# Optimization experiments

Hardware: AMD Instinct MI355X
Metric: run time of the kernel (lower is better)

The kernel has to match this reference:

```python
import jax, jax.numpy as jnp
import numpy as np

B, NQ, NK, D = 8, 2048, 2048, 1024

def setup_inputs() -> dict:
    key = jax.random.key(0)
    k1, k2, k3, k4, k5 = jax.random.split(key, 5)
    query_input = jax.random.normal(k1, (B, NQ, D), dtype=jnp.float32)
    key_input = jax.random.normal(k2, (B, NK, D), dtype=jnp.float32)
    s = 1.0 / np.sqrt(D)
    # nn.Linear(in,out,bias=False): y = x @ W.T, W shape (out,in)
    Wq = jax.random.uniform(k3, (D, D), dtype=jnp.float32, minval=-s, maxval=s)
    Wk = jax.random.uniform(k4, (D, D), dtype=jnp.float32, minval=-s, maxval=s)
    Wv = jax.random.uniform(k5, (D, D), dtype=jnp.float32, minval=-s, maxval=s)
    return {"query_input": query_input, "key_input": key_input,
            "Wq": Wq, "Wk": Wk, "Wv": Wv}

def reference(query_input, key_input, Wq, Wk, Wv):
    d = query_input.shape[-1]
    q = jnp.einsum('bnd,ed->bne', query_input, Wq)   # (b, n_q, d)
    k = jnp.einsum('bmd,ed->bme', key_input, Wk)     # (b, n_k, d)
    v = jnp.einsum('bnd,ed->bne', query_input, Wv)   # (b, n_q, d) -- value from query_input
    # scores: K @ Q^T -> (b, n_k, n_q), softmax over n_q
    a = jnp.einsum('bmd,bnd->bmn', k, q) / jnp.sqrt(jnp.float32(d))
    a = jax.nn.softmax(a, axis=-1)
    context = jnp.einsum('bmn,bnd->bmd', a, v)       # (b, n_k, d)
    return context + key_input
```

## Files before the change

### kernel.cpp

```cpp
#include <hip/hip_runtime.h>
#include <hip/hip_bf16.h>

using bf16 = __bf16;
typedef __bf16 bf16x8 __attribute__((ext_vector_type(8)));
typedef float f32x4 __attribute__((ext_vector_type(4)));

__device__ __forceinline__ void gload_lds16(const bf16* g, bf16* l) {
  __builtin_amdgcn_global_load_lds(
      (const __attribute__((address_space(1))) void*)g,
      (__attribute__((address_space(3))) void*)l, 16, 0, 0);
}

__global__ __launch_bounds__(256) void cvt_f32_bf16(const float* __restrict__ in,
                                                    bf16* __restrict__ out, int n) {
  int i = (blockIdx.x * 256 + threadIdx.x) * 8;
  if (i >= n) return;
  float4 f0 = *(const float4*)&in[i];
  float4 f1 = *(const float4*)&in[i + 4];
  bf16x8 o;
  o[0] = (bf16)f0.x; o[1] = (bf16)f0.y; o[2] = (bf16)f0.z; o[3] = (bf16)f0.w;
  o[4] = (bf16)f1.x; o[5] = (bf16)f1.y; o[6] = (bf16)f1.z; o[7] = (bf16)f1.w;
  *(bf16x8*)&out[i] = o;
}

template <int EPI>
__global__ __launch_bounds__(512, 2)
void gemm_bt(const bf16* __restrict__ A, const bf16* __restrict__ B,
             void* __restrict__ Cv, const float* __restrict__ Add,
             int K, int lda, int ldb, int ldc,
             long sA, long sB, long sC, long sAdd, float scale) {
  const int z = blockIdx.z;
  A += (long)z * sA;
  B += (long)z * sB;
  const int tid = threadIdx.x;
  const int lane = tid & 63;
  const int wave = tid >> 6;
  const int wr = wave >> 2;
  const int wc = wave & 3;
  const long brow = (long)blockIdx.x * 256;
  const long bcol = (long)blockIdx.y * 256;

  __shared__ bf16 lds[4][16384];

  f32x4 acc[8][4] = {};

  const int srow = tid >> 2;
  const int scg  = (tid & 3) ^ ((srow >> 1) & 3);
  const bf16* gA = A + (brow + srow) * (long)lda + scg * 8;
  const bf16* gB = B + (bcol + srow) * (long)ldb + scg * 8;
  const long a128 = (long)lda << 7;
  const long b128 = (long)ldb << 7;

  const int nk = K >> 5;

  auto stageA = [&](int t) {
    bf16* buf = lds[t & 3];
    const bf16* g = gA + (long)t * 32;
    gload_lds16(g,        buf + tid * 8);
    gload_lds16(g + a128, buf + 4096 + tid * 8);
  };
  auto stageB = [&](int t) {
    bf16* buf = lds[t & 3];
    const bf16* g = gB + (long)t * 32;
    gload_lds16(g,        buf + 8192 + tid * 8);
    gload_lds16(g + b128, buf + 12288 + tid * 8);
  };

  stageA(0); stageB(0);
  stageA(1); stageB(1);
  stageA(2); stageB(2);
  asm volatile("s_waitcnt vmcnt(8)" ::: "memory");
  __builtin_amdgcn_s_barrier();

  const int lk = lane >> 4;
  const int lr = lane & 15;

  for (int t = 0; t < nk; ++t) {
    bf16* buf = lds[t & 3];
    bf16x8 av[8], bv[4];
#pragma unroll
    for (int mi = 0; mi < 4; ++mi) {
      const int r = wr * 128 + mi * 16 + lr;
      av[mi] = *(const bf16x8*)&buf[r * 32 + ((lk ^ ((r >> 1) & 3)) << 3)];
    }
#pragma unroll
    for (int ni = 0; ni < 4; ++ni) {
      const int r = wc * 64 + ni * 16 + lr;
      bv[ni] = *(const bf16x8*)&buf[8192 + r * 32 + ((lk ^ ((r >> 1) & 3)) << 3)];
    }
    if (t + 3 < nk) stageA(t + 3);
    __builtin_amdgcn_s_setprio(1);
#pragma unroll
    for (int mi = 0; mi < 4; ++mi)
#pragma unroll
      for (int ni = 0; ni < 4; ++ni)
        acc[mi][ni] = __builtin_amdgcn_mfma_f32_16x16x32_bf16(av[mi], bv[ni],
                                                              acc[mi][ni], 0, 0, 0);
    __builtin_amdgcn_s_setprio(0);
    __builtin_amdgcn_s_barrier();
#pragma unroll
    for (int mi = 4; mi < 8; ++mi) {
      const int r = wr * 128 + mi * 16 + lr;
      av[mi] = *(const bf16x8*)&buf[r * 32 + ((lk ^ ((r >> 1) & 3)) << 3)];
    }
    if (t + 3 < nk) stageB(t + 3);
    __builtin_amdgcn_s_setprio(1);
#pragma unroll
    for (int mi = 4; mi < 8; ++mi)
#pragma unroll
      for (int ni = 0; ni < 4; ++ni)
        acc[mi][ni] = __builtin_amdgcn_mfma_f32_16x16x32_bf16(av[mi], bv[ni],
                                                              acc[mi][ni], 0, 0, 0);
    __builtin_amdgcn_s_setprio(0);
    if (t < nk - 3)       { asm volatile("s_waitcnt vmcnt(8)" ::: "memory"); }
    else if (t == nk - 3) { asm volatile("s_waitcnt vmcnt(4)" ::: "memory"); }
    else if (t == nk - 2) { asm volatile("s_waitcnt vmcnt(0)" ::: "memory"); }
    __builtin_amdgcn_s_barrier();
  }

  const int or0 = wr * 128 + ((lane >> 4) << 2);
  const int oc0 = wc * 64 + (lane & 15);
#pragma unroll
  for (int mi = 0; mi < 8; ++mi) {
#pragma unroll
    for (int ni = 0; ni < 4; ++ni) {
#pragma unroll
      for (int j = 0; j < 4; ++j) {
        const long row = brow + or0 + mi * 16 + j;
        const long col = bcol + oc0 + ni * 16;
        const float vres = acc[mi][ni][j] * scale;
        if constexpr (EPI == 0) {
          bf16* C = (bf16*)Cv + (long)z * sC;
          C[row * ldc + col] = (bf16)vres;
        } else {
          float* C = (float*)Cv + (long)z * sC;
          const float* Ad = Add + (long)z * sAdd;
          C[row * ldc + col] = vres + Ad[row * ldc + col];
        }
      }
    }
  }
}

__global__ __launch_bounds__(256) void softmax_rows(bf16* __restrict__ S) {
  const long row = blockIdx.x;
  bf16* p = S + row * 2048;
  const int tid = threadIdx.x;
  bf16x8 v = *(const bf16x8*)&p[tid * 8];
  float x[8];
  float m = -1e30f;
#pragma unroll
  for (int i = 0; i < 8; ++i) { x[i] = (float)v[i]; m = fmaxf(m, x[i]); }
#pragma unroll
  for (int off = 32; off > 0; off >>= 1) m = fmaxf(m, __shfl_xor(m, off, 64));
  __shared__ float red[4];
  __shared__ float red2[4];
  if ((tid & 63) == 0) red[tid >> 6] = m;
  __syncthreads();
  m = fmaxf(fmaxf(red[0], red[1]), fmaxf(red[2], red[3]));
  float e[8];
  float s = 0.f;
#pragma unroll
  for (int i = 0; i < 8; ++i) { e[i] = __expf(x[i] - m); s += e[i]; }
#pragma unroll
  for (int off = 32; off > 0; off >>= 1) s += __shfl_xor(s, off, 64);
  if ((tid & 63) == 0) red2[tid >> 6] = s;
  __syncthreads();
  s = red2[0] + red2[1] + red2[2] + red2[3];
  const float inv = 1.0f / s;
  bf16x8 o;
#pragma unroll
  for (int i = 0; i < 8; ++i) o[i] = (bf16)(e[i] * inv);
  *(bf16x8*)&p[tid * 8] = o;
}

extern "C" void kernel_launch(void* const* d_in, const int* in_sizes, int n_in,
                              void* d_out, int out_size, void* d_ws, size_t ws_size,
                              hipStream_t stream) {
  const float* q_in = (const float*)d_in[0];
  const float* k_in = (const float*)d_in[1];
  const float* Wq   = (const float*)d_in[2];
  const float* Wk   = (const float*)d_in[3];
  const float* Wv   = (const float*)d_in[4];
  float* out = (float*)d_out;
  char* ws = (char*)d_ws;

  bf16* qb  = (bf16*)(ws);
  bf16* kb  = (bf16*)(ws + 33554432);
  bf16* S   = (bf16*)(ws);
  bf16* Wqb = (bf16*)(ws + 67108864);
  bf16* Wkb = (bf16*)(ws + 69206016);
  bf16* Wvb = (bf16*)(ws + 71303168);
  bf16* Qp  = (bf16*)(ws + 73400320);
  bf16* Kp  = (bf16*)(ws + 106954752);
  bf16* Vpt = (bf16*)(ws + 140509184);

  cvt_f32_bf16<<<8192, 256, 0, stream>>>(q_in, qb, 16777216);
  cvt_f32_bf16<<<8192, 256, 0, stream>>>(k_in, kb, 16777216);
  cvt_f32_bf16<<<512, 256, 0, stream>>>(Wq, Wqb, 1048576);
  cvt_f32_bf16<<<512, 256, 0, stream>>>(Wk, Wkb, 1048576);
  cvt_f32_bf16<<<512, 256, 0, stream>>>(Wv, Wvb, 1048576);

  gemm_bt<0><<<dim3(64, 4, 1), 512, 0, stream>>>(
      qb, Wqb, Qp, nullptr, 1024, 1024, 1024, 1024, 0, 0, 0, 0, 1.0f);
  gemm_bt<0><<<dim3(64, 4, 1), 512, 0, stream>>>(
      kb, Wkb, Kp, nullptr, 1024, 1024, 1024, 1024, 0, 0, 0, 0, 1.0f);
  gemm_bt<0><<<dim3(4, 8, 8), 512, 0, stream>>>(
      Wvb, qb, Vpt, nullptr, 1024, 1024, 1024, 2048,
      0L, 2097152L, 2097152L, 0L, 1.0f);

  gemm_bt<0><<<dim3(8, 8, 8), 512, 0, stream>>>(
      Kp, Qp, S, nullptr, 1024, 1024, 1024, 2048,
      2097152L, 2097152L, 4194304L, 0L, 0.03125f);

  softmax_rows<<<16384, 256, 0, stream>>>(S);

  gemm_bt<2><<<dim3(8, 4, 8), 512, 0, stream>>>(
      S, Vpt, out, k_in, 2048, 2048, 2048, 1024,
      4194304L, 2097152L, 2097152L, 2097152L, 1.0f);
}
```

Before: 340.0 us.

## Fuse exp into score GEMM, defer softmax normalization, reschedule GEMM main loop

The score GEMM epilogue now writes exp(scaled score) directly with no max subtraction. A light row-sum kernel computes reciprocal sums, and the final GEMM multiplies by that inverse in its epilogue, so the separate softmax pass no longer rereads and rewrites S. The GEMM main loop is split into four finer LDS-read/MFMA phases with interleaved async loads, extra barriers and sched_barriers. Batched grids also get an XCD-aware block remap. Dropping the max subtraction risks overflow and precision loss if scores are large, and the extra barriers may add sync overhead.

After: 341.9 us. About the same (+0.6%).

```diff
diff --git a/kernel.cpp b/kernel.cpp
--- a/kernel.cpp
+++ b/kernel.cpp
@@ -27,18 +27,27 @@
 __global__ __launch_bounds__(512, 2)
 void gemm_bt(const bf16* __restrict__ A, const bf16* __restrict__ B,
              void* __restrict__ Cv, const float* __restrict__ Add,
+             const float* __restrict__ Inv,
              int K, int lda, int ldb, int ldc,
              long sA, long sB, long sC, long sAdd, float scale) {
-  const int z = blockIdx.z;
-  A += (long)z * sA;
-  B += (long)z * sB;
+  int bx = blockIdx.x, by = blockIdx.y, bz = blockIdx.z;
+  if (gridDim.z > 1) {
+    const int gx = gridDim.x, gxy = gx * gridDim.y;
+    const int nwg = gxy * gridDim.z;
+    int lin = bx + gx * by + gxy * bz;
+    lin = (lin & 7) * (nwg >> 3) + (lin >> 3);
+    bz = lin / gxy; const int rem = lin - bz * gxy;
+    by = rem / gx;  bx = rem - by * gx;
+  }
+  A += (long)bz * sA;
+  B += (long)bz * sB;
   const int tid = threadIdx.x;
   const int lane = tid & 63;
   const int wave = tid >> 6;
   const int wr = wave >> 2;
   const int wc = wave & 3;
-  const long brow = (long)blockIdx.x * 256;
-  const long bcol = (long)blockIdx.y * 256;
+  const long brow = (long)bx * 256;
+  const long bcol = (long)by * 256;
 
   __shared__ bf16 lds[4][16384];
 
@@ -53,64 +62,84 @@
 
   const int nk = K >> 5;
 
-  auto stageA = [&](int t) {
-    bf16* buf = lds[t & 3];
-    const bf16* g = gA + (long)t * 32;
-    gload_lds16(g,        buf + tid * 8);
-    gload_lds16(g + a128, buf + 4096 + tid * 8);
-  };
-  auto stageB = [&](int t) {
-    bf16* buf = lds[t & 3];
-    const bf16* g = gB + (long)t * 32;
-    gload_lds16(g,        buf + 8192 + tid * 8);
-    gload_lds16(g + b128, buf + 12288 + tid * 8);
-  };
-
-  stageA(0); stageB(0);
-  stageA(1); stageB(1);
-  stageA(2); stageB(2);
+  auto stageAlo = [&](int t) { gload_lds16(gA + (long)t * 32,        lds[t & 3] + tid * 8); };
+  auto stageAhi = [&](int t) { gload_lds16(gA + a128 + (long)t * 32, lds[t & 3] + 4096 + tid * 8); };
+  auto stageBlo = [&](int t) { gload_lds16(gB + (long)t * 32,        lds[t & 3] + 8192 + tid * 8); };
+  auto stageBhi = [&](int t) { gload_lds16(gB + b128 + (long)t * 32, lds[t & 3] + 12288 + tid * 8); };
+
+  stageAlo(0); stageAhi(0); stageBlo(0); stageBhi(0);
+  stageAlo(1); stageAhi(1); stageBlo(1); stageBhi(1);
+  stageAlo(2); stageAhi(2); stageBlo(2); stageBhi(2);
   asm volatile("s_waitcnt vmcnt(8)" ::: "memory");
   __builtin_amdgcn_s_barrier();
 
   const int lk = lane >> 4;
   const int lr = lane & 15;
+
+  auto rdA = [&](const bf16* buf, int mi) -> bf16x8 {
+    const int r = wr * 128 + mi * 16 + lr;
+    return *(const bf16x8*)&buf[r * 32 + ((lk ^ ((r >> 1) & 3)) << 3)];
+  };
+  auto rdB = [&](const bf16* buf, int ni) -> bf16x8 {
+    const int r = wc * 64 + ni * 16 + lr;
+    return *(const bf16x8*)&buf[8192 + r * 32 + ((lk ^ ((r >> 1) & 3)) << 3)];
+  };
 
   for (int t = 0; t < nk; ++t) {
     bf16* buf = lds[t & 3];
     bf16x8 av[8], bv[4];
 #pragma unroll
-    for (int mi = 0; mi < 4; ++mi) {
-      const int r = wr * 128 + mi * 16 + lr;
-      av[mi] = *(const bf16x8*)&buf[r * 32 + ((lk ^ ((r >> 1) & 3)) << 3)];
-    }
-#pragma unroll
-    for (int ni = 0; ni < 4; ++ni) {
-      const int r = wc * 64 + ni * 16 + lr;
-      bv[ni] = *(const bf16x8*)&buf[8192 + r * 32 + ((lk ^ ((r >> 1) & 3)) << 3)];
-    }
-    if (t + 3 < nk) stageA(t + 3);
+    for (int mi = 0; mi < 4; ++mi) av[mi] = rdA(buf, mi);
+#pragma unroll
+    for (int ni = 0; ni < 2; ++ni) bv[ni] = rdB(buf, ni);
+    if (t + 3 < nk) stageAlo(t + 3);
+    __builtin_amdgcn_s_barrier();
+    asm volatile("s_waitcnt lgkmcnt(0)" ::: "memory");
+    __builtin_amdgcn_sched_barrier(0);
     __builtin_amdgcn_s_setprio(1);
 #pragma unroll
     for (int mi = 0; mi < 4; ++mi)
 #pragma unroll
-      for (int ni = 0; ni < 4; ++ni)
-        acc[mi][ni] = __builtin_amdgcn_mfma_f32_16x16x32_bf16(av[mi], bv[ni],
-                                                              acc[mi][ni], 0, 0, 0);
-    __builtin_amdgcn_s_setprio(0);
-    __builtin_amdgcn_s_barrier();
-#pragma unroll
-    for (int mi = 4; mi < 8; ++mi) {
-      const int r = wr * 128 + mi * 16 + lr;
-      av[mi] = *(const bf16x8*)&buf[r * 32 + ((lk ^ ((r >> 1) & 3)) << 3)];
-    }
-    if (t + 3 < nk) stageB(t + 3);
+      for (int ni = 0; ni < 2; ++ni)
+        acc[mi][ni] = __builtin_amdgcn_mfma_f32_16x16x32_bf16(av[mi], bv[ni], acc[mi][ni], 0, 0, 0);
+    __builtin_amdgcn_s_setprio(0);
+    __builtin_amdgcn_s_barrier();
+#pragma unroll
+    for (int ni = 2; ni < 4; ++ni) bv[ni] = rdB(buf, ni);
+    if (t + 3 < nk) stageAhi(t + 3);
+    __builtin_amdgcn_s_barrier();
+    asm volatile("s_waitcnt lgkmcnt(0)" ::: "memory");
+    __builtin_amdgcn_sched_barrier(0);
+    __builtin_amdgcn_s_setprio(1);
+#pragma unroll
+    for (int mi = 0; mi < 4; ++mi)
+#pragma unroll
+      for (int ni = 2; ni < 4; ++ni)
+        acc[mi][ni] = __builtin_amdgcn_mfma_f32_16x16x32_bf16(av[mi], bv[ni], acc[mi][ni], 0, 0, 0);
+    __builtin_amdgcn_s_setprio(0);
+    __builtin_amdgcn_s_barrier();
+#pragma unroll
+    for (int mi = 4; mi < 8; ++mi) av[mi] = rdA(buf, mi);
+    if (t + 3 < nk) stageBlo(t + 3);
+    __builtin_amdgcn_s_barrier();
+    asm volatile("s_waitcnt lgkmcnt(0)" ::: "memory");
+    __builtin_amdgcn_sched_barrier(0);
     __builtin_amdgcn_s_setprio(1);
 #pragma unroll
     for (int mi = 4; mi < 8; ++mi)
 #pragma unroll
-      for (int ni = 0; ni < 4; ++ni)
-        acc[mi][ni] = __builtin_amdgcn_mfma_f32_16x16x32_bf16(av[mi], bv[ni],
-                                                              acc[mi][ni], 0, 0, 0);
+      for (int ni = 2; ni < 4; ++ni)
+        acc[mi][ni] = __builtin_amdgcn_mfma_f32_16x16x32_bf16(av[mi], bv[ni], acc[mi][ni], 0, 0, 0);
+    __builtin_amdgcn_s_setprio(0);
+    __builtin_amdgcn_s_barrier();
+    if (t + 3 < nk) stageBhi(t + 3);
+    __builtin_amdgcn_s_barrier();
+    __builtin_amdgcn_s_setprio(1);
+#pragma unroll
+    for (int mi = 4; mi < 8; ++mi)
+#pragma unroll
+      for (int ni = 0; ni < 2; ++ni)
+        acc[mi][ni] = __builtin_amdgcn_mfma_f32_16x16x32_bf16(av[mi], bv[ni], acc[mi][ni], 0, 0, 0);
     __builtin_amdgcn_s_setprio(0);
     if (t < nk - 3)       { asm volatile("s_waitcnt vmcnt(8)" ::: "memory"); }
     else if (t == nk - 3) { asm volatile("s_waitcnt vmcnt(4)" ::: "memory"); }
@@ -128,50 +157,38 @@
       for (int j = 0; j < 4; ++j) {
         const long row = brow + or0 + mi * 16 + j;
         const long col = bcol + oc0 + ni * 16;
-        const float vres = acc[mi][ni][j] * scale;
         if constexpr (EPI == 0) {
-          bf16* C = (bf16*)Cv + (long)z * sC;
-          C[row * ldc + col] = (bf16)vres;
+          bf16* C = (bf16*)Cv + (long)bz * sC;
+          C[row * ldc + col] = (bf16)(acc[mi][ni][j] * scale);
+        } else if constexpr (EPI == 1) {
+          bf16* C = (bf16*)Cv + (long)bz * sC;
+          C[row * ldc + col] = (bf16)__expf(acc[mi][ni][j] * scale);
         } else {
-          float* C = (float*)Cv + (long)z * sC;
-          const float* Ad = Add + (long)z * sAdd;
-          C[row * ldc + col] = vres + Ad[row * ldc + col];
+          float* C = (float*)Cv + (long)bz * sC;
+          const float* Ad = Add + (long)bz * sAdd;
+          const float* iv = Inv + (long)bz * 2048;
+          C[row * ldc + col] = acc[mi][ni][j] * iv[row] + Ad[row * ldc + col];
         }
       }
     }
   }
 }
 
-__global__ __launch_bounds__(256) void softmax_rows(bf16* __restrict__ S) {
+__global__ __launch_bounds__(256) void rowsum_inv(const bf16* __restrict__ E,
+                                                  float* __restrict__ inv) {
   const long row = blockIdx.x;
-  bf16* p = S + row * 2048;
+  const bf16* p = E + row * 2048;
   const int tid = threadIdx.x;
   bf16x8 v = *(const bf16x8*)&p[tid * 8];
-  float x[8];
-  float m = -1e30f;
-#pragma unroll
-  for (int i = 0; i < 8; ++i) { x[i] = (float)v[i]; m = fmaxf(m, x[i]); }
-#pragma unroll
-  for (int off = 32; off > 0; off >>= 1) m = fmaxf(m, __shfl_xor(m, off, 64));
+  float s = 0.f;
+#pragma unroll
+  for (int i = 0; i < 8; ++i) s += (float)v[i];
+#pragma unroll
+  for (int off = 32; off > 0; off >>= 1) s += __shfl_xor(s, off, 64);
   __shared__ float red[4];
-  __shared__ float red2[4];
-  if ((tid & 63) == 0) red[tid >> 6] = m;
+  if ((tid & 63) == 0) red[tid >> 6] = s;
   __syncthreads();
-  m = fmaxf(fmaxf(red[0], red[1]), fmaxf(red[2], red[3]));
-  float e[8];
-  float s = 0.f;
-#pragma unroll
-  for (int i = 0; i < 8; ++i) { e[i] = __expf(x[i] - m); s += e[i]; }
-#pragma unroll
-  for (int off = 32; off > 0; off >>= 1) s += __shfl_xor(s, off, 64);
-  if ((tid & 63) == 0) red2[tid >> 6] = s;
-  __syncthreads();
-  s = red2[0] + red2[1] + red2[2] + red2[3];
-  const float inv = 1.0f / s;
-  bf16x8 o;
-#pragma unroll
-  for (int i = 0; i < 8; ++i) o[i] = (bf16)(e[i] * inv);
-  *(bf16x8*)&p[tid * 8] = o;
+  if (tid == 0) inv[row] = 1.0f / (red[0] + red[1] + red[2] + red[3]);
 }
 
 extern "C" void kernel_launch(void* const* d_in, const int* in_sizes, int n_in,
@@ -189,6 +206,7 @@
   bf16* kb  = (bf16*)(ws + 33554432);
   bf16* S   = (bf16*)(ws);
   bf16* Wqb = (bf16*)(ws + 67108864);
+  float* inv = (float*)(ws + 67108864);
   bf16* Wkb = (bf16*)(ws + 69206016);
   bf16* Wvb = (bf16*)(ws + 71303168);
   bf16* Qp  = (bf16*)(ws + 73400320);
@@ -202,20 +220,20 @@
   cvt_f32_bf16<<<512, 256, 0, stream>>>(Wv, Wvb, 1048576);
 
   gemm_bt<0><<<dim3(64, 4, 1), 512, 0, stream>>>(
-      qb, Wqb, Qp, nullptr, 1024, 1024, 1024, 1024, 0, 0, 0, 0, 1.0f);
+      qb, Wqb, Qp, nullptr, nullptr, 1024, 1024, 1024, 1024, 0, 0, 0, 0, 1.0f);
   gemm_bt<0><<<dim3(64, 4, 1), 512, 0, stream>>>(
-      kb, Wkb, Kp, nullptr, 1024, 1024, 1024, 1024, 0, 0, 0, 0, 1.0f);
+      kb, Wkb, Kp, nullptr, nullptr, 1024, 1024, 1024, 1024, 0, 0, 0, 0, 1.0f);
   gemm_bt<0><<<dim3(4, 8, 8), 512, 0, stream>>>(
-      Wvb, qb, Vpt, nullptr, 1024, 1024, 1024, 2048,
+      Wvb, qb, Vpt, nullptr, nullptr, 1024, 1024, 1024, 2048,
       0L, 2097152L, 2097152L, 0L, 1.0f);
 
-  gemm_bt<0><<<dim3(8, 8, 8), 512, 0, stream>>>(
-      Kp, Qp, S, nullptr, 1024, 1024, 1024, 2048,
+  gemm_bt<1><<<dim3(8, 8, 8), 512, 0, stream>>>(
+      Kp, Qp, S, nullptr, nullptr, 1024, 1024, 1024, 2048,
       2097152L, 2097152L, 4194304L, 0L, 0.03125f);
 
-  softmax_rows<<<16384, 256, 0, stream>>>(S);
+  rowsum_inv<<<16384, 256, 0, stream>>>(S, inv);
 
   gemm_bt<2><<<dim3(8, 4, 8), 512, 0, stream>>>(
-      S, Vpt, out, k_in, 2048, 2048, 2048, 1024,
+      S, Vpt, out, k_in, inv, 2048, 2048, 2048, 1024,
       4194304L, 2097152L, 2097152L, 2097152L, 1.0f);
 }
```
